# Kernel optimization log

Measured on AMD Instinct MI355X. Metric: run time of the kernel, lower is better.

The kernel has to match this reference:

```python
import jax, jax.numpy as jnp
import numpy as np

N = 50000        # nodes
E = 800000       # edges
H = 256          # hidden_dim == output_dim
L = 5            # num_layers
NUM_ATOM_F = 9   # OGB atom categorical features
NUM_BOND_F = 3   # OGB bond categorical features
ATOM_VOCAB = 64
BOND_VOCAB = 8
G = 128          # num graphs in batch
BN_EPS = 1e-5


def setup_inputs() -> dict:
    key = jax.random.key(0)
    ks = jax.random.split(key, 24)
    s = 0.02
    inp = {
        "x_feat": jax.random.randint(ks[0], (N, NUM_ATOM_F), 0, ATOM_VOCAB),
        "edge_index": jax.random.randint(ks[1], (2, E), 0, N),
        "edge_attr_raw": jax.random.randint(ks[2], (E, NUM_BOND_F), 0, BOND_VOCAB),
        "batch": jnp.sort(jax.random.randint(ks[3], (N,), 0, G)),
        "atom_emb": s * jax.random.normal(ks[4], (NUM_ATOM_F, ATOM_VOCAB, H), jnp.float32),
        "bond_emb": s * jax.random.normal(ks[5], (NUM_BOND_F, BOND_VOCAB, H), jnp.float32),
        # per-layer GINEConv MLP: Linear(H,H) -> BN -> relu -> Linear(H,H) -> relu
        "W1": s * jax.random.normal(ks[6], (L, H, H), jnp.float32),
        "b1": jnp.zeros((L, H), jnp.float32),
        "g1": jnp.ones((L, H), jnp.float32),
        "be1": jnp.zeros((L, H), jnp.float32),
        "W2": s * jax.random.normal(ks[7], (L, H, H), jnp.float32),
        "b2": jnp.zeros((L, H), jnp.float32),
        # outer per-layer BN
        "g2": jnp.ones((L, H), jnp.float32),
        "be2": jnp.zeros((L, H), jnp.float32),
        # output head: Linear -> BN -> relu -> Linear
        "outW1": s * jax.random.normal(ks[8], (H, H), jnp.float32),
        "outb1": jnp.zeros((H,), jnp.float32),
        "outg": jnp.ones((H,), jnp.float32),
        "outbe": jnp.zeros((H,), jnp.float32),
        "outW2": s * jax.random.normal(ks[9], (H, H), jnp.float32),
        "outb2": jnp.zeros((H,), jnp.float32),
    }
    return inp


def _bn(x, g, b):
    mu = jnp.mean(x, axis=0)
    var = jnp.var(x, axis=0)
    return (x - mu) * jax.lax.rsqrt(var + BN_EPS) * g + b


def reference(x_feat, edge_index, edge_attr_raw, batch,
              atom_emb, bond_emb, W1, b1, g1, be1, W2, b2, g2, be2,
              outW1, outb1, outg, outbe, outW2, outb2):
    # Atom/Bond encoders: sum of per-feature embeddings
    x = sum(atom_emb[f][x_feat[:, f]] for f in range(NUM_ATOM_F))        # [N,H]
    e = sum(bond_emb[f][edge_attr_raw[:, f]] for f in range(NUM_BOND_F))  # [E,H]
    src, dst = edge_index[0], edge_index[1]

    for i in range(L):
        # GINEConv: (1+eps)*x + sum_j relu(x_j + e_ij), eps=0
        m = jax.nn.relu(x[src] + e)                       # [E,H]
        agg = jax.ops.segment_sum(m, dst, num_segments=N)  # [N,H]
        h = x + agg
        h = jax.nn.relu(_bn(h @ W1[i] + b1[i], g1[i], be1[i]))
        h = jax.nn.relu(h @ W2[i] + b2[i])
        x = jax.nn.relu(_bn(h, g2[i], be2[i]))

    # output head + global_add_pool
    h = jax.nn.relu(_bn(x @ outW1 + outb1, outg, outbe))
    h = h @ outW2 + outb2
    return jax.ops.segment_sum(h, batch, num_segments=G)   # [G,H]
```

## Files before the change

### kernel.cpp

```cpp
#include <hip/hip_runtime.h>
#include <hip/hip_bf16.h>

#define NN 50000
#define EE 800000
#define HH 256
#define GG 128
#define LL 5
#define NCHUNK 196
#define BN_EPS 1e-5f

typedef __attribute__((ext_vector_type(8))) short short8_t;
typedef __attribute__((ext_vector_type(4))) float f32x4;
typedef __hip_bfloat16 bf16;

#define AS1 __attribute__((address_space(1)))
#define AS3 __attribute__((address_space(3)))

__device__ __forceinline__ float bf2f(unsigned short u) {
    unsigned int i = ((unsigned int)u) << 16;
    float f;
    __builtin_memcpy(&f, &i, 4);
    return f;
}
__device__ __forceinline__ unsigned short f2bf(float f) {
    bf16 h = __float2bfloat16(f);
    unsigned short u;
    __builtin_memcpy(&u, &h, 2);
    return u;
}

__global__ __launch_bounds__(256) void k_encode(const int* __restrict__ xf,
                                                const float* __restrict__ atom_emb,
                                                bf16* __restrict__ x) {
    int n = blockIdx.x, h = threadIdx.x;
    float s = 0.f;
#pragma unroll
    for (int f = 0; f < 9; ++f) {
        int v = xf[n * 9 + f];
        s += atom_emb[((size_t)f * 64 + v) * HH + h];
    }
    x[(size_t)n * HH + h] = __float2bfloat16(s);
}

__global__ __launch_bounds__(256) void k_combo(const float* __restrict__ bond_emb,
                                               bf16* __restrict__ table) {
    int c = blockIdx.x, h = threadIdx.x;
    float v = bond_emb[(size_t)((c >> 6) & 7) * HH + h]
            + bond_emb[(size_t)(8 + ((c >> 3) & 7)) * HH + h]
            + bond_emb[(size_t)(16 + (c & 7)) * HH + h];
    table[(size_t)c * HH + h] = __float2bfloat16(v);
}

__global__ __launch_bounds__(256) void k_prepw(const float* __restrict__ W1,
                                               const float* __restrict__ W2,
                                               const float* __restrict__ oW1,
                                               const float* __restrict__ oW2,
                                               bf16* __restrict__ out) {
    int z = blockIdx.z;
    const float* src = (z < 5) ? W1 + (size_t)z * 65536
                     : (z < 10) ? W2 + (size_t)(z - 5) * 65536
                     : (z == 10) ? oW1 : oW2;
    bf16* dst = out + (size_t)z * 65536;
    __shared__ float tile[32][33];
    int kt = blockIdx.y * 32, nt = blockIdx.x * 32;
    int tx = threadIdx.x, ty = threadIdx.y;
    for (int i = ty; i < 32; i += 8) tile[i][tx] = src[(size_t)(kt + i) * 256 + nt + tx];
    __syncthreads();
    for (int i = ty; i < 32; i += 8)
        dst[(size_t)(nt + i) * 256 + kt + tx] = __float2bfloat16(tile[tx][i]);
}

__global__ __launch_bounds__(256) void k_hist(const int* __restrict__ ei, int* __restrict__ deg) {
    int e = blockIdx.x * 256 + threadIdx.x;
    if (e < EE) atomicAdd(&deg[ei[EE + e]], 1);
}

__global__ __launch_bounds__(256) void k_scan_a(const int* __restrict__ deg, int* __restrict__ ro,
                                                int* __restrict__ bsum) {
    __shared__ int sm[256];
    int b = blockIdx.x, t = threadIdx.x;
    int idx = b * 256 + t;
    int v = (idx < NN) ? deg[idx] : 0;
    sm[t] = v;
    __syncthreads();
    for (int off = 1; off < 256; off <<= 1) {
        int add = (t >= off) ? sm[t - off] : 0;
        __syncthreads();
        sm[t] += add;
        __syncthreads();
    }
    if (idx <= NN) ro[idx] = sm[t] - v;
    if (t == 255) bsum[b] = sm[255];
}

__global__ __launch_bounds__(256) void k_scan_b(int* __restrict__ bsum) {
    __shared__ int sm[256];
    int t = threadIdx.x;
    int v = (t < NCHUNK) ? bsum[t] : 0;
    sm[t] = v;
    __syncthreads();
    for (int off = 1; off < 256; off <<= 1) {
        int add = (t >= off) ? sm[t - off] : 0;
        __syncthreads();
        sm[t] += add;
        __syncthreads();
    }
    if (t < NCHUNK) bsum[t] = sm[t] - v;
}

__global__ __launch_bounds__(256) void k_scan_c(int* __restrict__ ro, const int* __restrict__ bsum,
                                                int* __restrict__ cursor) {
    int b = blockIdx.x, t = threadIdx.x;
    int idx = b * 256 + t;
    if (idx <= NN) {
        int val = ro[idx] + bsum[b];
        ro[idx] = val;
        if (idx < NN) cursor[idx] = val;
    }
}

__global__ __launch_bounds__(256) void k_scatter(const int* __restrict__ ei,
                                                 const int* __restrict__ attr,
                                                 int* __restrict__ cursor,
                                                 int2* __restrict__ ebuf) {
    int e = blockIdx.x * 256 + threadIdx.x;
    if (e < EE) {
        int d = ei[EE + e];
        int c = (attr[e * 3] << 6) | (attr[e * 3 + 1] << 3) | attr[e * 3 + 2];
        int pos = atomicAdd(&cursor[d], 1);
        ebuf[pos] = make_int2(ei[e], c);
    }
}

__global__ __launch_bounds__(256) void k_bnrelu(bf16* __restrict__ t,
                                                const float* __restrict__ sIn,
                                                const float* __restrict__ qIn,
                                                const float* __restrict__ gIn,
                                                const float* __restrict__ beIn,
                                                float invN) {
    int grp = threadIdx.x >> 6;
    int lane = threadIdx.x & 63;
    int h4 = lane * 4;
    float4 s4 = *(const float4*)(sIn + h4);
    float4 q4 = *(const float4*)(qIn + h4);
    float4 g4 = *(const float4*)(gIn + h4);
    float4 b4 = *(const float4*)(beIn + h4);
    float4 cav, cbv;
#define COEF(C)                                                 \
    { float mu = s4.C * invN;                                   \
      float var = fmaf(-mu, mu, q4.C * invN);                   \
      float a = g4.C * rsqrtf(var + BN_EPS);                    \
      cav.C = a; cbv.C = fmaf(-mu, a, b4.C); }
    COEF(x) COEF(y) COEF(z) COEF(w)
#undef COEF
    int n = blockIdx.x * 4 + grp;
    if (n >= NN) return;
    ushort4 v = *(const ushort4*)(t + (size_t)n * HH + h4);
    ushort4 o;
    o.x = f2bf(fmaxf(fmaf(bf2f(v.x), cav.x, cbv.x), 0.f));
    o.y = f2bf(fmaxf(fmaf(bf2f(v.y), cav.y, cbv.y), 0.f));
    o.z = f2bf(fmaxf(fmaf(bf2f(v.z), cav.z, cbv.z), 0.f));
    o.w = f2bf(fmaxf(fmaf(bf2f(v.w), cav.w, cbv.w), 0.f));
    *(ushort4*)(t + (size_t)n * HH + h4) = o;
}

__global__ __launch_bounds__(256) void k_aggregate(const bf16* __restrict__ u,
                                                   const int* __restrict__ ro,
                                                   const int2* __restrict__ eb,
                                                   const bf16* __restrict__ combo,
                                                   bf16* __restrict__ aggout) {
    int wid = threadIdx.x >> 6;
    int lane = threadIdx.x & 63;
    int half = lane >> 5;
    int sl = lane & 31;
    int n = blockIdx.x * 4 + wid;
    if (n >= NN) return;
    int h8 = sl * 8;
    float p0[8] = {0.f, 0.f, 0.f, 0.f, 0.f, 0.f, 0.f, 0.f};
    float p1[8] = {0.f, 0.f, 0.f, 0.f, 0.f, 0.f, 0.f, 0.f};
    int e0 = ro[n], e1 = ro[n + 1];
    int j = e0;
#define ACCUM(P, xs, cs)                                                       \
    {                                                                          \
        unsigned int xw[4] = {xs.x, xs.y, xs.z, xs.w};                         \
        unsigned int cw[4] = {cs.x, cs.y, cs.z, cs.w};                         \
        _Pragma("unroll") for (int q = 0; q < 4; ++q) {                        \
            float xlo = __uint_as_float(xw[q] << 16);                          \
            float xhi = __uint_as_float(xw[q] & 0xffff0000u);                  \
            float clo = __uint_as_float(cw[q] << 16);                          \
            float chi = __uint_as_float(cw[q] & 0xffff0000u);                  \
            P[2 * q] += fmaxf(xlo + clo, 0.f);                                 \
            P[2 * q + 1] += fmaxf(xhi + chi, 0.f);                             \
        }                                                                      \
    }
    for (; j + 4 <= e1; j += 4) {
        int2 rA = eb[j + half];
        int2 rB = eb[j + 2 + half];
        uint4 xA = *(const uint4*)(u + (size_t)rA.x * HH + h8);
        uint4 cA = *(const uint4*)(combo + ((size_t)rA.y << 8) + h8);
        uint4 xB = *(const uint4*)(u + (size_t)rB.x * HH + h8);
        uint4 cB = *(const uint4*)(combo + ((size_t)rB.y << 8) + h8);
        ACCUM(p0, xA, cA);
        ACCUM(p1, xB, cB);
    }
    for (; j < e1; j += 2) {
        int idx = j + half;
        bool v = idx < e1;
        int2 r = eb[v ? idx : e0];
        uint4 xA = *(const uint4*)(u + (size_t)r.x * HH + h8);
        uint4 cA = *(const uint4*)(combo + ((size_t)r.y << 8) + h8);
        if (v) ACCUM(p0, xA, cA);
    }
#undef ACCUM
#pragma unroll
    for (int i = 0; i < 8; ++i) {
        p0[i] += p1[i];
        p0[i] += __shfl_xor(p0[i], 32);
    }
    if (half == 0) {
        uint4 tv = *(const uint4*)(u + (size_t)n * HH + h8);
        unsigned int tw[4] = {tv.x, tv.y, tv.z, tv.w};
        unsigned int ow[4];
#pragma unroll
        for (int q = 0; q < 4; ++q) {
            float tlo = __uint_as_float(tw[q] << 16);
            float thi = __uint_as_float(tw[q] & 0xffff0000u);
            ow[q] = (unsigned int)f2bf(p0[2 * q] + tlo)
                  | ((unsigned int)f2bf(p0[2 * q + 1] + thi) << 16);
        }
        *(uint4*)(aggout + (size_t)n * HH + h8) = make_uint4(ow[0], ow[1], ow[2], ow[3]);
    }
}

__global__ __launch_bounds__(512, 4) void k_gemmF(const bf16* __restrict__ A,
                                                  const bf16* __restrict__ Wt,
                                                  const float* __restrict__ bias,
                                                  bf16* __restrict__ Out,
                                                  int M,
                                                  float* __restrict__ ssum,
                                                  float* __restrict__ ssq) {
    __shared__ uint4 Lb[2][1024];
    const int t = threadIdx.x;
    const int lane = t & 63;
    const int w = t >> 6;
    const int wr = w >> 2, wc = w & 3;
    const int m0 = blockIdx.x * 128;
    const int lhi = lane >> 4, llo = lane & 15;

    const int bcol = wc * 64 + lane;
    const bf16* bptr = Wt + (size_t)bcol * HH + wr * 8;

    size_t abase[4];
#pragma unroll
    for (int m = 0; m < 4; ++m)
        abase[m] = (size_t)(m0 + wr * 64 + m * 16 + llo) * HH + lhi * 8;

    f32x4 acc[4][4] = {};
    uint4 ar[4], nar[4];

#define STAGE_B(c, kb)                                                                        \
    _Pragma("unroll") for (int q = 0; q < 2; ++q) {                                           \
        __builtin_amdgcn_global_load_lds((const AS1 void*)(bptr + (kb) + q * 16),             \
                                         (AS3 void*)&Lb[c][q * 512 + w * 64], 16, 0, 0);      \
    }

    STAGE_B(0, 0);
#pragma unroll
    for (int m = 0; m < 4; ++m) ar[m] = *(const uint4*)(A + abase[m]);
    __syncthreads();

    int c = 0;
    for (int step = 0; step < 8; ++step) {
        const int kn = (step + 1) * 32;
        if (step < 7) {
            STAGE_B(c ^ 1, kn);
#pragma unroll
            for (int m = 0; m < 4; ++m) nar[m] = *(const uint4*)(A + abase[m] + kn);
        }
        short8_t af[4], bfv[4];
#pragma unroll
        for (int m = 0; m < 4; ++m) __builtin_memcpy(&af[m], &ar[m], 16);
#pragma unroll
        for (int n = 0; n < 4; ++n)
            bfv[n] = *(const short8_t*)&Lb[c][lhi * 256 + wc * 64 + n * 16 + llo];
#pragma unroll
        for (int m = 0; m < 4; ++m)
#pragma unroll
            for (int n = 0; n < 4; ++n)
                acc[m][n] = __builtin_amdgcn_mfma_f32_16x16x32_bf16(af[m], bfv[n], acc[m][n], 0, 0, 0);
        if (step < 7) {
#pragma unroll
            for (int m = 0; m < 4; ++m) ar[m] = nar[m];
        }
        __syncthreads();
        c ^= 1;
    }
#undef STAGE_B

    float bias_n[4];
    int col_n[4];
#pragma unroll
    for (int n = 0; n < 4; ++n) {
        col_n[n] = wc * 64 + n * 16 + llo;
        bias_n[n] = bias[col_n[n]];
    }
    float ps[4] = {0.f, 0.f, 0.f, 0.f}, pq[4] = {0.f, 0.f, 0.f, 0.f};
#pragma unroll
    for (int m = 0; m < 4; ++m) {
#pragma unroll
        for (int j = 0; j < 4; ++j) {
            int row = m0 + wr * 64 + m * 16 + lhi * 4 + j;
            bool valid = row < M;
#pragma unroll
            for (int n = 0; n < 4; ++n) {
                float v = acc[m][n][j] + bias_n[n];
                if (valid) {
                    Out[(size_t)row * HH + col_n[n]] = __float2bfloat16(v);
                    ps[n] += v;
                    pq[n] = fmaf(v, v, pq[n]);
                }
            }
        }
    }
#pragma unroll
    for (int n = 0; n < 4; ++n) {
        float s = ps[n];
        s += __shfl_xor(s, 16);
        s += __shfl_xor(s, 32);
        float q = pq[n];
        q += __shfl_xor(q, 16);
        q += __shfl_xor(q, 32);
        if (lhi == 0) {
            atomicAdd(&ssum[col_n[n]], s);
            atomicAdd(&ssq[col_n[n]], q);
        }
    }
}

struct GLds {
    uint4 a[2][512];
    uint4 b[2][1024];
    float ca[256], cb[256];
};

__device__ __forceinline__ uint4 xchunk(uint4 u, const float* ca, const float* cb, int k0) {
    float4 ca0 = *(const float4*)(ca + k0);
    float4 ca1 = *(const float4*)(ca + k0 + 4);
    float4 cb0 = *(const float4*)(cb + k0);
    float4 cb1 = *(const float4*)(cb + k0 + 4);
    float cav[8] = {ca0.x, ca0.y, ca0.z, ca0.w, ca1.x, ca1.y, ca1.z, ca1.w};
    float cbv[8] = {cb0.x, cb0.y, cb0.z, cb0.w, cb1.x, cb1.y, cb1.z, cb1.w};
    unsigned int s[4] = {u.x, u.y, u.z, u.w};
#pragma unroll
    for (int p = 0; p < 4; ++p) {
        float lo = bf2f((unsigned short)(s[p] & 0xffffu));
        float hi = bf2f((unsigned short)(s[p] >> 16));
        lo = fmaxf(fmaf(lo, cav[2 * p], cbv[2 * p]), 0.f);
        hi = fmaxf(fmaf(hi, cav[2 * p + 1], cbv[2 * p + 1]), 0.f);
        s[p] = (unsigned int)f2bf(lo) | ((unsigned int)f2bf(hi) << 16);
    }
    return make_uint4(s[0], s[1], s[2], s[3]);
}

template <bool POOL>
__global__ __launch_bounds__(512, 4) void k_gemmT(const bf16* __restrict__ A,
                                                  const bf16* __restrict__ Wt,
                                                  const float* __restrict__ bias,
                                                  bf16* __restrict__ Out,
                                                  int M, int do_relu,
                                                  const float* __restrict__ sIn,
                                                  const float* __restrict__ qIn,
                                                  const float* __restrict__ gIn,
                                                  const float* __restrict__ beIn,
                                                  float invN,
                                                  float* __restrict__ ssum,
                                                  float* __restrict__ ssq,
                                                  const int* __restrict__ pbatch,
                                                  float* __restrict__ pout) {
    __shared__ GLds L;
    const int t = threadIdx.x;
    const int lane = t & 63;
    const int w = t >> 6;
    const int wr = w >> 2, wc = w & 3;
    const int m0 = blockIdx.x * 128;
    const int lhi = lane >> 4, llo = lane & 15;

    if (t < 256) {
        float mu = sIn[t] * invN;
        float var = fmaf(-mu, mu, qIn[t] * invN);
        float a = gIn[t] * rsqrtf(var + BN_EPS);
        L.ca[t] = a;
        L.cb[t] = fmaf(-mu, a, beIn[t]);
    }
    __syncthreads();

    const int arow_i = t & 127, akg = t >> 7;
    const bf16* aptr = A + (size_t)(m0 + arow_i) * HH + akg * 8;
    const int bcol = wc * 64 + lane;
    const bf16* bptr = Wt + (size_t)bcol * HH + wr * 8;

    f32x4 acc[4][4] = {};
    uint4 areg, anext;

#define STAGE_B(c, kb)                                                                        \
    _Pragma("unroll") for (int q = 0; q < 2; ++q) {                                           \
        __builtin_amdgcn_global_load_lds((const AS1 void*)(bptr + (kb) + q * 16),             \
                                         (AS3 void*)&L.b[c][q * 512 + w * 64], 16, 0, 0);     \
    }

    STAGE_B(0, 0);
    areg = *(const uint4*)(aptr + 0);
    L.a[0][t] = xchunk(areg, L.ca, L.cb, akg * 8);
    __syncthreads();

    int c = 0;
    for (int step = 0; step < 8; ++step) {
        const int kn = (step + 1) * 32;
        if (step < 7) {
            STAGE_B(c ^ 1, kn);
            anext = *(const uint4*)(aptr + kn);
        }
        short8_t af[4], bfv[4];
#pragma unroll
        for (int m = 0; m < 4; ++m)
            af[m] = *(const short8_t*)&L.a[c][lhi * 128 + wr * 64 + m * 16 + llo];
#pragma unroll
        for (int n = 0; n < 4; ++n)
            bfv[n] = *(const short8_t*)&L.b[c][lhi * 256 + wc * 64 + n * 16 + llo];
#pragma unroll
        for (int m = 0; m < 4; ++m)
#pragma unroll
            for (int n = 0; n < 4; ++n)
                acc[m][n] = __builtin_amdgcn_mfma_f32_16x16x32_bf16(af[m], bfv[n], acc[m][n], 0, 0, 0);
        if (step < 7)
            L.a[c ^ 1][t] = xchunk(anext, L.ca, L.cb, kn + akg * 8);
        __syncthreads();
        c ^= 1;
    }
#undef STAGE_B

    float bias_n[4];
    int col_n[4];
#pragma unroll
    for (int n = 0; n < 4; ++n) {
        col_n[n] = wc * 64 + n * 16 + llo;
        bias_n[n] = bias[col_n[n]];
    }

    if (POOL) {
        int gcur = -1;
        float pacc[4] = {0.f, 0.f, 0.f, 0.f};
#pragma unroll
        for (int m = 0; m < 4; ++m) {
#pragma unroll
            for (int j = 0; j < 4; ++j) {
                int row = m0 + wr * 64 + m * 16 + lhi * 4 + j;
                if (row < M) {
                    int g = pbatch[row];
                    if (g != gcur) {
                        if (gcur >= 0) {
#pragma unroll
                            for (int n = 0; n < 4; ++n)
                                atomicAdd(&pout[(size_t)gcur * HH + col_n[n]], pacc[n]);
                        }
                        gcur = g;
#pragma unroll
                        for (int n = 0; n < 4; ++n) pacc[n] = 0.f;
                    }
#pragma unroll
                    for (int n = 0; n < 4; ++n)
                        pacc[n] += acc[m][n][j] + bias_n[n];
                }
            }
        }
        if (gcur >= 0) {
#pragma unroll
            for (int n = 0; n < 4; ++n)
                atomicAdd(&pout[(size_t)gcur * HH + col_n[n]], pacc[n]);
        }
        return;
    }

    float ps[4] = {0.f, 0.f, 0.f, 0.f}, pq[4] = {0.f, 0.f, 0.f, 0.f};
#pragma unroll
    for (int m = 0; m < 4; ++m) {
#pragma unroll
        for (int j = 0; j < 4; ++j) {
            int row = m0 + wr * 64 + m * 16 + lhi * 4 + j;
            bool valid = row < M;
#pragma unroll
            for (int n = 0; n < 4; ++n) {
                float v = acc[m][n][j] + bias_n[n];
                if (do_relu) v = fmaxf(v, 0.f);
                if (valid) {
                    Out[(size_t)row * HH + col_n[n]] = __float2bfloat16(v);
                    ps[n] += v;
                    pq[n] = fmaf(v, v, pq[n]);
                }
            }
        }
    }

    if (ssum) {
#pragma unroll
        for (int n = 0; n < 4; ++n) {
            float s = ps[n];
            s += __shfl_xor(s, 16);
            s += __shfl_xor(s, 32);
            float q = pq[n];
            q += __shfl_xor(q, 16);
            q += __shfl_xor(q, 32);
            if (lhi == 0) {
                atomicAdd(&ssum[col_n[n]], s);
                atomicAdd(&ssq[col_n[n]], q);
            }
        }
    }
}

static size_t align256(size_t v) { return (v + 255) & ~(size_t)255; }

extern "C" void kernel_launch(void* const* d_in, const int* in_sizes, int n_in,
                              void* d_out, int out_size, void* d_ws, size_t ws_size,
                              hipStream_t stream) {
    const int* x_feat = (const int*)d_in[0];
    const int* ei = (const int*)d_in[1];
    const int* attr = (const int*)d_in[2];
    const int* batch = (const int*)d_in[3];
    const float* atom_emb = (const float*)d_in[4];
    const float* bond_emb = (const float*)d_in[5];
    const float* W1 = (const float*)d_in[6];
    const float* b1 = (const float*)d_in[7];
    const float* g1 = (const float*)d_in[8];
    const float* be1 = (const float*)d_in[9];
    const float* W2 = (const float*)d_in[10];
    const float* b2 = (const float*)d_in[11];
    const float* g2 = (const float*)d_in[12];
    const float* be2 = (const float*)d_in[13];
    const float* outW1 = (const float*)d_in[14];
    const float* outb1 = (const float*)d_in[15];
    const float* outg = (const float*)d_in[16];
    const float* outbe = (const float*)d_in[17];
    const float* outW2 = (const float*)d_in[18];
    const float* outb2 = (const float*)d_in[19];
    float* out = (float*)d_out;

    char* ws = (char*)d_ws;
    const size_t BUF_STRIDE = align256((size_t)NN * HH * 2 + 131072);
    bf16* bufA = (bf16*)ws;
    bf16* bufB = (bf16*)(ws + BUF_STRIDE);
    bf16* bufC = (bf16*)(ws + 2 * BUF_STRIDE);
    char* p = ws + 3 * BUF_STRIDE;
    int2* ebuf = (int2*)p;            p += align256((size_t)EE * sizeof(int2));
    int* deg = (int*)p;
    float* stats = (float*)(p + (size_t)NN * sizeof(int));
    const size_t ZERO_BYTES = (size_t)NN * sizeof(int) + 11 * 512 * sizeof(float);
    p += align256(ZERO_BYTES);
    int* ro = (int*)p;                p += align256((size_t)(NN + 1) * sizeof(int));
    int* cursor = (int*)p;            p += align256((size_t)NN * sizeof(int));
    int* bsum = (int*)p;              p += align256(256 * sizeof(int));
    bf16* combo = (bf16*)p;           p += align256((size_t)512 * HH * sizeof(bf16));
    bf16* wbuf = (bf16*)p;            p += align256((size_t)12 * 65536 * sizeof(bf16));

    const float invN = 1.0f / (float)NN;
    const int EBLK = (EE + 255) / 256;
    const int GBLK = (NN + 127) / 128;
    const int AGG_GRID = (NN + 3) / 4;
    const int BNR_GRID = (NN + 3) / 4;

    hipMemsetAsync(deg, 0, ZERO_BYTES, stream);
    hipMemsetAsync(d_out, 0, (size_t)GG * HH * sizeof(float), stream);
    k_hist<<<EBLK, 256, 0, stream>>>(ei, deg);
    k_scan_a<<<NCHUNK, 256, 0, stream>>>(deg, ro, bsum);
    k_scan_b<<<1, 256, 0, stream>>>(bsum);
    k_scan_c<<<NCHUNK, 256, 0, stream>>>(ro, bsum, cursor);
    k_scatter<<<EBLK, 256, 0, stream>>>(ei, attr, cursor, ebuf);
    k_combo<<<512, 256, 0, stream>>>(bond_emb, combo);
    k_prepw<<<dim3(8, 8, 12), dim3(32, 8), 0, stream>>>(W1, W2, outW1, outW2, wbuf);
    k_encode<<<NN, 256, 0, stream>>>(x_feat, atom_emb, bufA);

    for (int l = 0; l < LL; ++l) {
        float* s1 = stats + (size_t)(2 * l) * 512;
        float* q1 = s1 + 256;
        float* s2 = stats + (size_t)(2 * l + 1) * 512;
        float* q2 = s2 + 256;
        if (l > 0) {
            float* sp = stats + (size_t)(2 * l - 1) * 512;
            k_bnrelu<<<BNR_GRID, 256, 0, stream>>>(bufA, sp, sp + 256,
                                                   g2 + (size_t)(l - 1) * HH,
                                                   be2 + (size_t)(l - 1) * HH, invN);
        }
        k_aggregate<<<AGG_GRID, 256, 0, stream>>>(bufA, ro, ebuf, combo, bufB);
        k_gemmF<<<GBLK, 512, 0, stream>>>(bufB, wbuf + (size_t)l * 65536,
                                          b1 + (size_t)l * HH, bufC, NN, s1, q1);
        k_gemmT<false><<<GBLK, 512, 0, stream>>>(bufC, wbuf + (size_t)(5 + l) * 65536,
                                                 b2 + (size_t)l * HH, bufA, NN, 1,
                                                 s1, q1, g1 + (size_t)l * HH,
                                                 be1 + (size_t)l * HH, invN, s2, q2,
                                                 nullptr, nullptr);
    }

    float* sP = stats + (size_t)9 * 512;
    float* sH = stats + (size_t)10 * 512;
    float* qH = sH + 256;
    k_gemmT<false><<<GBLK, 512, 0, stream>>>(bufA, wbuf + (size_t)10 * 65536, outb1,
                                             bufB, NN, 0, sP, sP + 256,
                                             g2 + (size_t)4 * HH, be2 + (size_t)4 * HH,
                                             invN, sH, qH, nullptr, nullptr);
    k_gemmT<true><<<GBLK, 512, 0, stream>>>(bufB, wbuf + (size_t)11 * 65536, outb2,
                                            bufC, NN, 0, sH, qH, outg, outbe,
                                            invN, nullptr, nullptr, batch, out);
}
```

Before: 965.0 us.

## Pack edge records to 32 bits and restructure gemm tiling with half-K weight staging

Edge records shrink from int2 to a single 32-bit word, with the source node in the low 16 bits and the bond combo in the high bits. This halves edge-buffer traffic in the aggregation kernel. The fused GEMM now uses a 4x2 wave grid where each wave computes 32 rows by 128 columns. Weights are staged into LDS in two 128-K phases instead of double-buffered 32-K steps, which cuts barriers and reuses A fragments across more columns. Because NN is 50000, node indices above 65535 do not occur, but a 16-bit index field silently truncates any node id of 65536 or more, so the packing depends on the graph size. The scatter kernel also processes two edges per thread.

```diff
diff --git a/kernel.cpp b/kernel.cpp
--- a/kernel.cpp
+++ b/kernel.cpp
@@ -122,13 +122,17 @@
 __global__ __launch_bounds__(256) void k_scatter(const int* __restrict__ ei,
                                                  const int* __restrict__ attr,
                                                  int* __restrict__ cursor,
-                                                 int2* __restrict__ ebuf) {
-    int e = blockIdx.x * 256 + threadIdx.x;
-    if (e < EE) {
-        int d = ei[EE + e];
-        int c = (attr[e * 3] << 6) | (attr[e * 3 + 1] << 3) | attr[e * 3 + 2];
-        int pos = atomicAdd(&cursor[d], 1);
-        ebuf[pos] = make_int2(ei[e], c);
+                                                 unsigned int* __restrict__ ebuf) {
+    int e0 = blockIdx.x * 512 + threadIdx.x;
+#pragma unroll
+    for (int r = 0; r < 2; ++r) {
+        int e = e0 + r * 256;
+        if (e < EE) {
+            int d = ei[EE + e];
+            unsigned int c = (unsigned int)((attr[e * 3] << 6) | (attr[e * 3 + 1] << 3) | attr[e * 3 + 2]);
+            int pos = atomicAdd(&cursor[d], 1);
+            ebuf[pos] = (c << 16) | (unsigned int)ei[e];
+        }
     }
 }
 
@@ -166,7 +170,7 @@
 
 __global__ __launch_bounds__(256) void k_aggregate(const bf16* __restrict__ u,
                                                    const int* __restrict__ ro,
-                                                   const int2* __restrict__ eb,
+                                                   const unsigned int* __restrict__ eb,
                                                    const bf16* __restrict__ combo,
                                                    bf16* __restrict__ aggout) {
     int wid = threadIdx.x >> 6;
@@ -194,21 +198,21 @@
         }                                                                      \
     }
     for (; j + 4 <= e1; j += 4) {
-        int2 rA = eb[j + half];
-        int2 rB = eb[j + 2 + half];
-        uint4 xA = *(const uint4*)(u + (size_t)rA.x * HH + h8);
-        uint4 cA = *(const uint4*)(combo + ((size_t)rA.y << 8) + h8);
-        uint4 xB = *(const uint4*)(u + (size_t)rB.x * HH + h8);
-        uint4 cB = *(const uint4*)(combo + ((size_t)rB.y << 8) + h8);
+        unsigned int rA = eb[j + half];
+        unsigned int rB = eb[j + 2 + half];
+        uint4 xA = *(const uint4*)(u + (size_t)(rA & 0xffffu) * HH + h8);
+        uint4 cA = *(const uint4*)(combo + ((size_t)(rA >> 16) << 8) + h8);
+        uint4 xB = *(const uint4*)(u + (size_t)(rB & 0xffffu) * HH + h8);
+        uint4 cB = *(const uint4*)(combo + ((size_t)(rB >> 16) << 8) + h8);
         ACCUM(p0, xA, cA);
         ACCUM(p1, xB, cB);
     }
     for (; j < e1; j += 2) {
         int idx = j + half;
         bool v = idx < e1;
-        int2 r = eb[v ? idx : e0];
-        uint4 xA = *(const uint4*)(u + (size_t)r.x * HH + h8);
-        uint4 cA = *(const uint4*)(combo + ((size_t)r.y << 8) + h8);
+        unsigned int r = eb[v ? idx : e0];
+        uint4 xA = *(const uint4*)(u + (size_t)(r & 0xffffu) * HH + h8);
+        uint4 cA = *(const uint4*)(combo + ((size_t)(r >> 16) << 8) + h8);
         if (v) ACCUM(p0, xA, cA);
     }
 #undef ACCUM
@@ -239,80 +243,75 @@
                                                   int M,
                                                   float* __restrict__ ssum,
                                                   float* __restrict__ ssq) {
-    __shared__ uint4 Lb[2][1024];
+    __shared__ uint4 Lb[4096];
     const int t = threadIdx.x;
     const int lane = t & 63;
     const int w = t >> 6;
-    const int wr = w >> 2, wc = w & 3;
+    const int wr = w >> 1, wc = w & 1;
     const int m0 = blockIdx.x * 128;
     const int lhi = lane >> 4, llo = lane & 15;
 
-    const int bcol = wc * 64 + lane;
-    const bf16* bptr = Wt + (size_t)bcol * HH + wr * 8;
-
-    size_t abase[4];
-#pragma unroll
-    for (int m = 0; m < 4; ++m)
-        abase[m] = (size_t)(m0 + wr * 64 + m * 16 + llo) * HH + lhi * 8;
-
-    f32x4 acc[4][4] = {};
-    uint4 ar[4], nar[4];
-
-#define STAGE_B(c, kb)                                                                        \
-    _Pragma("unroll") for (int q = 0; q < 2; ++q) {                                           \
-        __builtin_amdgcn_global_load_lds((const AS1 void*)(bptr + (kb) + q * 16),             \
-                                         (AS3 void*)&Lb[c][q * 512 + w * 64], 16, 0, 0);      \
-    }
-
-    STAGE_B(0, 0);
-#pragma unroll
-    for (int m = 0; m < 4; ++m) ar[m] = *(const uint4*)(A + abase[m]);
-    __syncthreads();
-
-    int c = 0;
-    for (int step = 0; step < 8; ++step) {
-        const int kn = (step + 1) * 32;
-        if (step < 7) {
-            STAGE_B(c ^ 1, kn);
-#pragma unroll
-            for (int m = 0; m < 4; ++m) nar[m] = *(const uint4*)(A + abase[m] + kn);
-        }
-        short8_t af[4], bfv[4];
-#pragma unroll
-        for (int m = 0; m < 4; ++m) __builtin_memcpy(&af[m], &ar[m], 16);
-#pragma unroll
-        for (int n = 0; n < 4; ++n)
-            bfv[n] = *(const short8_t*)&Lb[c][lhi * 256 + wc * 64 + n * 16 + llo];
-#pragma unroll
-        for (int m = 0; m < 4; ++m)
-#pragma unroll
-            for (int n = 0; n < 4; ++n)
-                acc[m][n] = __builtin_amdgcn_mfma_f32_16x16x32_bf16(af[m], bfv[n], acc[m][n], 0, 0, 0);
-        if (step < 7) {
-#pragma unroll
-            for (int m = 0; m < 4; ++m) ar[m] = nar[m];
+    const int scol = ((w & 3) << 6) + lane;
+    const int skg0 = w >> 2;
+    const int sbase = ((w & 3) << 6);
+
+    const size_t arow0 = (size_t)(m0 + wr * 32 + llo) * HH + lhi * 8;
+    const size_t arow1 = arow0 + (size_t)16 * HH;
+
+    f32x4 acc[2][8] = {};
+    uint4 a0 = *(const uint4*)(A + arow0);
+    uint4 a1 = *(const uint4*)(A + arow1);
+    uint4 n0_, n1_;
+
+    for (int ph = 0; ph < 2; ++ph) {
+        if (ph) __syncthreads();
+#pragma unroll
+        for (int i = 0; i < 8; ++i) {
+            const int kgl = skg0 + i * 2;
+            const bf16* src = Wt + (size_t)scol * HH + ph * 128 + kgl * 8;
+            __builtin_amdgcn_global_load_lds((const AS1 void*)src,
+                                             (AS3 void*)&Lb[kgl * 256 + sbase], 16, 0, 0);
         }
         __syncthreads();
-        c ^= 1;
-    }
-#undef STAGE_B
-
-    float bias_n[4];
-    int col_n[4];
-#pragma unroll
-    for (int n = 0; n < 4; ++n) {
-        col_n[n] = wc * 64 + n * 16 + llo;
+#pragma unroll
+        for (int s = 0; s < 4; ++s) {
+            const int gs = ph * 4 + s;
+            if (gs < 7) {
+                n0_ = *(const uint4*)(A + arow0 + (gs + 1) * 32);
+                n1_ = *(const uint4*)(A + arow1 + (gs + 1) * 32);
+            }
+            short8_t af[2], bfv[8];
+            __builtin_memcpy(&af[0], &a0, 16);
+            __builtin_memcpy(&af[1], &a1, 16);
+#pragma unroll
+            for (int n = 0; n < 8; ++n)
+                bfv[n] = *(const short8_t*)&Lb[(s * 4 + lhi) * 256 + wc * 128 + n * 16 + llo];
+#pragma unroll
+            for (int m = 0; m < 2; ++m)
+#pragma unroll
+                for (int n = 0; n < 8; ++n)
+                    acc[m][n] = __builtin_amdgcn_mfma_f32_16x16x32_bf16(af[m], bfv[n], acc[m][n], 0, 0, 0);
+            if (gs < 7) { a0 = n0_; a1 = n1_; }
+        }
+    }
+
+    float bias_n[8];
+    int col_n[8];
+#pragma unroll
+    for (int n = 0; n < 8; ++n) {
+        col_n[n] = wc * 128 + n * 16 + llo;
         bias_n[n] = bias[col_n[n]];
     }
-    float ps[4] = {0.f, 0.f, 0.f, 0.f}, pq[4] = {0.f, 0.f, 0.f, 0.f};
-#pragma unroll
-    for (int m = 0; m < 4; ++m) {
+    float ps[8] = {0.f, 0.f, 0.f, 0.f, 0.f, 0.f, 0.f, 0.f};
+    float pq[8] = {0.f, 0.f, 0.f, 0.f, 0.f, 0.f, 0.f, 0.f};
+#pragma unroll
+    for (int m = 0; m < 2; ++m) {
 #pragma unroll
         for (int j = 0; j < 4; ++j) {
-            int row = m0 + wr * 64 + m * 16 + lhi * 4 + j;
+            int row = m0 + wr * 32 + m * 16 + lhi * 4 + j;
             bool valid = row < M;
 #pragma unroll
-            for (int n = 0; n < 4; ++n) {
+            for (int n = 0; n < 8; ++n) {
                 float v = acc[m][n][j] + bias_n[n];
                 if (valid) {
                     Out[(size_t)row * HH + col_n[n]] = __float2bfloat16(v);
@@ -323,7 +322,7 @@
         }
     }
 #pragma unroll
-    for (int n = 0; n < 4; ++n) {
+    for (int n = 0; n < 8; ++n) {
         float s = ps[n];
         s += __shfl_xor(s, 16);
         s += __shfl_xor(s, 32);
@@ -551,7 +550,7 @@
     bf16* bufB = (bf16*)(ws + BUF_STRIDE);
     bf16* bufC = (bf16*)(ws + 2 * BUF_STRIDE);
     char* p = ws + 3 * BUF_STRIDE;
-    int2* ebuf = (int2*)p;            p += align256((size_t)EE * sizeof(int2));
+    unsigned int* ebuf = (unsigned int*)p;  p += align256((size_t)EE * sizeof(unsigned int));
     int* deg = (int*)p;
     float* stats = (float*)(p + (size_t)NN * sizeof(int));
     const size_t ZERO_BYTES = (size_t)NN * sizeof(int) + 11 * 512 * sizeof(float);
@@ -574,7 +573,7 @@
     k_scan_a<<<NCHUNK, 256, 0, stream>>>(deg, ro, bsum);
     k_scan_b<<<1, 256, 0, stream>>>(bsum);
     k_scan_c<<<NCHUNK, 256, 0, stream>>>(ro, bsum, cursor);
-    k_scatter<<<EBLK, 256, 0, stream>>>(ei, attr, cursor, ebuf);
+    k_scatter<<<(EE + 511) / 512, 256, 0, stream>>>(ei, attr, cursor, ebuf);
     k_combo<<<512, 256, 0, stream>>>(bond_emb, combo);
     k_prepw<<<dim3(8, 8, 12), dim3(32, 8), 0, stream>>>(W1, W2, outW1, outW2, wbuf);
     k_encode<<<NN, 256, 0, stream>>>(x_feat, atom_emb, bufA);
```

New measurement: 1.005 ms. 1.04x slower.
